# Kernel tuning notes

Measured on AMD Instinct MI355X. Metric: run time of the kernel, lower is better.

The kernel has to match this reference:

```python
import jax, jax.numpy as jnp
import numpy as np

B, S, D, H = 2, 2048, 1024, 16
DK = D // H  # 64


def setup_inputs() -> dict:
    key = jax.random.key(0)
    ks = jax.random.split(key, 4)
    scale = 1.0 / np.sqrt(D)
    return {
        "q_input": jax.random.normal(ks[0], (B, S, D), dtype=jnp.float32),
        "W_q": jax.random.normal(ks[1], (D, D), dtype=jnp.float32) * scale,
        "b_q": jnp.zeros((D,), dtype=jnp.float32),
        "W_k": jax.random.normal(ks[2], (D, D), dtype=jnp.float32) * scale,
        "b_k": jnp.zeros((D,), dtype=jnp.float32),
        "W_v": jax.random.normal(ks[3], (D, D), dtype=jnp.float32) * scale,
        "b_v": jnp.zeros((D,), dtype=jnp.float32),
    }


def reference(q_input, W_q, b_q, W_k, b_k, W_v, b_v):
    # Self-attention: k_input and v_input default to q_input in the torch module.
    # nn.Linear computes x @ W.T + b
    q = q_input @ W_q.T + b_q
    k = q_input @ W_k.T + b_k
    v = q_input @ W_v.T + b_v

    # [B,S,D] -> [B,H,S,DK]
    def split_heads(x):
        return x.reshape(B, S, H, DK).transpose(0, 2, 1, 3)

    qh, kh, vh = split_heads(q), split_heads(k), split_heads(v)

    # scores [B,H,S,S]; causal mask added BEFORE scaling (as in source; -inf invariant)
    scores = jnp.einsum("bhqd,bhkd->bhqk", qh, kh)
    causal = jnp.tril(jnp.ones((S, S), dtype=bool))
    scores = jnp.where(causal[None, None], scores, -jnp.inf)
    scores = scores / jnp.sqrt(jnp.float32(DK))
    probs = jax.nn.softmax(scores, axis=-1)
    z = jnp.einsum("bhqk,bhkd->bhqd", probs, vh)  # [B,H,S,DK]
    # [B,H,S,DK] -> [B,S,H,DK] -> [B,S,D]
    return z.transpose(0, 2, 1, 3).reshape(B, S, D)
```

## Files before the change

kernel.cpp:

```cpp
#include <hip/hip_runtime.h>
#include <hip/hip_bf16.h>
#include <stdint.h>

typedef __attribute__((ext_vector_type(8))) short short8;
typedef __attribute__((ext_vector_type(4))) short short4v;
typedef __attribute__((ext_vector_type(4))) float f32x4;

#define B_ 2
#define S_ 2048
#define D_ 1024
#define H_ 16
#define DK_ 64
#define M_ (B_*S_)

#define WS_QKV   0
#define WS_XB    12582912
#define WS_WB    16777216

#define QSCALE (0.125f * 1.44269504088896f)

#define GLL16(g, l) __builtin_amdgcn_global_load_lds( \
    (const __attribute__((address_space(1))) void*)(g), \
    (__attribute__((address_space(3))) void*)(l), 16, 0, 0)

#define WAIT_VM0 asm volatile("s_waitcnt vmcnt(0)" ::: "memory")
#define BARRIER_RAW asm volatile("s_barrier" ::: "memory")

static __device__ __forceinline__ short f2bf(float f){
  union { float f; unsigned u; } x; x.f = f;
  unsigned r = x.u + 0x7fff + ((x.u >> 16) & 1);
  return (short)(r >> 16);
}

__global__ __launch_bounds__(256) void cvt_bf16(
    const float* __restrict__ X,  const float* __restrict__ Wq,
    const float* __restrict__ Wk, const float* __restrict__ Wv,
    short* __restrict__ ws)
{
  const int z = blockIdx.z;
  const float* src; short* dst; int n;
  if (z == 0)      { src = X;  dst = ws + WS_XB;               n = M_*D_; }
  else if (z == 1) { src = Wq; dst = ws + WS_WB;               n = D_*D_; }
  else if (z == 2) { src = Wk; dst = ws + WS_WB + D_*D_;       n = D_*D_; }
  else             { src = Wv; dst = ws + WS_WB + 2*(D_*D_);   n = D_*D_; }
  const int stride = gridDim.x * blockDim.x * 4;
  for (int i = (blockIdx.x * blockDim.x + threadIdx.x) * 4; i < n; i += stride) {
    float4 v = *(const float4*)(src + i);
    short4v o;
    o.x = f2bf(v.x); o.y = f2bf(v.y); o.z = f2bf(v.z); o.w = f2bf(v.w);
    *(short4v*)(dst + i) = o;
  }
}

__global__ __launch_bounds__(256, 3) void qkv_gemm(
    const short* __restrict__ ws_in,
    const float* __restrict__ bq, const float* __restrict__ bk,
    const float* __restrict__ bv, short* __restrict__ qkv)
{
  const int z = blockIdx.z;
  const short* X  = ws_in + WS_XB;
  const short* Wm = ws_in + WS_WB + (size_t)z * (D_*D_);
  const float* bias = (z==0) ? bq : (z==1) ? bk : bv;
  short* out = qkv + (size_t)z * (M_*D_);

  __shared__ short lds[17408];

  const int t = threadIdx.x;
  const int w = t >> 6, lane = t & 63;
  const int quad = lane >> 4, l16 = lane & 15;
  const int wm = w & 1, wn = w >> 1;
  const int m0 = blockIdx.y * 128, n0 = blockIdx.x * 128;

  const int lr = lane >> 2, lc = lane & 3;
  const int csrc = lc ^ (lr & 3);
  const size_t arow0 = (size_t)(m0 + w*16     + lr) * D_ + csrc*8;
  const size_t arow1 = (size_t)(m0 + (w+4)*16 + lr) * D_ + csrc*8;
  const size_t brow0 = (size_t)(n0 + w*16     + lr) * D_ + csrc*8;
  const size_t brow1 = (size_t)(n0 + (w+4)*16 + lr) * D_ + csrc*8;

  f32x4 acc[4][4];
  #pragma unroll
  for (int i=0;i<4;i++)
    #pragma unroll
    for (int j=0;j<4;j++) acc[i][j] = (f32x4){0.f,0.f,0.f,0.f};

  GLL16(X  + arow0, lds + (w*16)*32);
  GLL16(X  + arow1, lds + ((w+4)*16)*32);
  GLL16(Wm + brow0, lds + 8192 + (w*16)*32);
  GLL16(Wm + brow1, lds + 8192 + ((w+4)*16)*32);

  const int ca = quad ^ (l16 & 3);
  int cur = 0;
  for (int kk = 0; kk < 32; kk++) {
    WAIT_VM0;
    BARRIER_RAW;
    const int nxt = cur ^ 1;
    if (kk < 31) {
      const int ko = (kk+1)*32;
      short* An = lds + nxt*4096;
      short* Bn = lds + 8192 + nxt*4096;
      GLL16(X  + arow0 + ko, An + (w*16)*32);
      GLL16(X  + arow1 + ko, An + ((w+4)*16)*32);
      GLL16(Wm + brow0 + ko, Bn + (w*16)*32);
      GLL16(Wm + brow1 + ko, Bn + ((w+4)*16)*32);
    }
    const short* Ac = lds + cur*4096;
    const short* Bc = lds + 8192 + cur*4096;
    short8 af[4], bfr[4];
    #pragma unroll
    for (int mt=0;mt<4;mt++)
      af[mt] = *(const short8*)(Ac + (wm*64 + mt*16 + l16)*32 + ca*8);
    #pragma unroll
    for (int nt=0;nt<4;nt++)
      bfr[nt] = *(const short8*)(Bc + (wn*64 + nt*16 + l16)*32 + ca*8);
    if (z != 2) {
      #pragma unroll
      for (int mt=0;mt<4;mt++)
        #pragma unroll
        for (int nt=0;nt<4;nt++)
          acc[mt][nt] = __builtin_amdgcn_mfma_f32_16x16x32_bf16(af[mt], bfr[nt], acc[mt][nt], 0,0,0);
    } else {
      #pragma unroll
      for (int nt=0;nt<4;nt++)
        #pragma unroll
        for (int mt=0;mt<4;mt++)
          acc[nt][mt] = __builtin_amdgcn_mfma_f32_16x16x32_bf16(bfr[nt], af[mt], acc[nt][mt], 0,0,0);
    }
    cur = nxt;
  }

  __syncthreads();

  if (z != 2) {
    const float scale = (z==0) ? QSCALE : 1.0f;
    #pragma unroll
    for (int nt=0;nt<4;nt++){
      const int col_l = wn*64 + nt*16 + l16;
      const float bvv = bias[n0 + col_l];
      #pragma unroll
      for (int mt=0;mt<4;mt++)
        #pragma unroll
        for (int i=0;i<4;i++){
          const int row_l = wm*64 + mt*16 + quad*4 + i;
          lds[row_l*136 + col_l] = f2bf((acc[mt][nt][i] + bvv) * scale);
        }
    }
    __syncthreads();
    #pragma unroll
    for (int k=0;k<8;k++){
      const int cid = k*256 + t;
      const int row = cid >> 4, cc = cid & 15;
      short8 vv = *(const short8*)(lds + row*136 + cc*8);
      const int m = m0 + row, bidx = m >> 11, s = m & 2047;
      const int n = n0 + cc*8, h = n >> 6, dd = n & 63;
      *(short8*)(out + (((size_t)(bidx*H_ + h))*S_ + s)*DK_ + dd) = vv;
    }
  } else {
    #pragma unroll
    for (int nt=0;nt<4;nt++)
      #pragma unroll
      for (int i=0;i<4;i++){
        const int n_l = wn*64 + nt*16 + quad*4 + i;
        const float bvv = bias[n0 + n_l];
        #pragma unroll
        for (int mt=0;mt<4;mt++){
          const int m_l = wm*64 + mt*16 + l16;
          lds[n_l*136 + m_l] = f2bf(acc[nt][mt][i] + bvv);
        }
      }
    __syncthreads();
    #pragma unroll
    for (int k=0;k<8;k++){
      const int cid = k*256 + t;
      const int rowN = cid >> 4, cc = cid & 15;
      short8 vv = *(const short8*)(lds + rowN*136 + cc*8);
      const int n = n0 + rowN, h = n >> 6, dd = n & 63;
      const int m = m0 + cc*8, bidx = m >> 11, s0 = m & 2047;
      *(short8*)(out + (((size_t)(bidx*H_ + h))*DK_ + dd)*S_ + s0) = vv;
    }
  }
}

__global__ __launch_bounds__(256, 2) void attn(
    const short* __restrict__ qkv, float* __restrict__ out)
{
  const int bh = blockIdx.y;
  const int qt = (gridDim.x - 1) - blockIdx.x;
  const short* Q  = qkv + (size_t)bh * (S_*DK_);
  const short* K  = Q + (size_t)(M_*D_);
  const short* VT = qkv + (size_t)(2*M_*D_) + (size_t)bh * (DK_*S_);

  __shared__ short Qs[8192];
  __shared__ short Kbuf[2][4096];
  __shared__ short Vbuf[2][4096];
  __shared__ short Ps[8192];

  const int t = threadIdx.x;
  const int w = t >> 6, lane = t & 63;
  const int quad = lane >> 4, l16 = lane & 15;
  const int sw = l16 & 7;
  const int lr = lane >> 3, lc = lane & 7;
  const int csrc = lc ^ lr;

  #pragma unroll
  for (int p=0;p<4;p++){
    const int rb = (p*4 + w)*8;
    GLL16(Q + (size_t)(qt*128 + rb + lr)*DK_ + csrc*8, Qs + rb*64);
  }
  {
    #pragma unroll
    for (int j=0;j<2;j++){
      const int rb = (j*4 + w)*8;
      GLL16(K  + (size_t)(rb + lr)*DK_ + csrc*8, &Kbuf[0][0] + rb*64);
      GLL16(VT + (size_t)(rb + lr)*S_  + csrc*8, &Vbuf[0][0] + rb*64);
    }
  }

  f32x4 o[2][4];
  float lsum[2][4];
  #pragma unroll
  for (int mt=0;mt<2;mt++){
    #pragma unroll
    for (int nd=0;nd<4;nd++) o[mt][nd] = (f32x4){0.f,0.f,0.f,0.f};
    #pragma unroll
    for (int i=0;i<4;i++) lsum[mt][i] = 0.f;
  }

  short8 aq[2][2];
  const int nkt = 2*qt + 2;
  int cur = 0;
  for (int kt = 0; kt < nkt; kt++){
    WAIT_VM0;
    BARRIER_RAW;
    const int nxt = cur ^ 1;
    if (kt + 1 < nkt) {
      const int kb2 = (kt+1)*64;
      short* Kn = &Kbuf[nxt][0];
      short* Vn = &Vbuf[nxt][0];
      #pragma unroll
      for (int j=0;j<2;j++){
        const int rb = (j*4 + w)*8;
        GLL16(K  + (size_t)(kb2 + rb + lr)*DK_ + csrc*8, Kn + rb*64);
        GLL16(VT + (size_t)(rb + lr)*S_ + kb2 + csrc*8,  Vn + rb*64);
      }
    }
    if (kt == 0) {
      #pragma unroll
      for (int kc=0;kc<2;kc++){
        const int xch = (kc*4 + quad) ^ sw;
        #pragma unroll
        for (int mt=0;mt<2;mt++)
          aq[kc][mt] = *(const short8*)(Qs + (w*32 + mt*16 + l16)*64 + xch*8);
      }
    }
    const short* Kc = &Kbuf[cur][0];
    const short* Vc = &Vbuf[cur][0];
    const int kb = kt*64;

    f32x4 sc[2][4];
    #pragma unroll
    for (int mt=0;mt<2;mt++)
      #pragma unroll
      for (int ntk=0;ntk<4;ntk++) sc[mt][ntk] = (f32x4){0.f,0.f,0.f,0.f};
    #pragma unroll
    for (int kc=0;kc<2;kc++){
      const int xch = (kc*4 + quad) ^ sw;
      short8 bk8[4];
      #pragma unroll
      for (int ntk=0;ntk<4;ntk++)
        bk8[ntk] = *(const short8*)(Kc + (ntk*16 + l16)*64 + xch*8);
      #pragma unroll
      for (int mt=0;mt<2;mt++)
        #pragma unroll
        for (int ntk=0;ntk<4;ntk++)
          sc[mt][ntk] = __builtin_amdgcn_mfma_f32_16x16x32_bf16(aq[kc][mt], bk8[ntk], sc[mt][ntk], 0,0,0);
    }

    const int q0w = qt*128 + w*32;
    if (kb + 63 > q0w) {
      #pragma unroll
      for (int mt=0;mt<2;mt++)
        #pragma unroll
        for (int ntk=0;ntk<4;ntk++)
          #pragma unroll
          for (int i=0;i<4;i++){
            const int qg = q0w + mt*16 + quad*4 + i;
            const int kg = kb + ntk*16 + l16;
            if (kg > qg) sc[mt][ntk][i] = -3.0e38f;
          }
    }

    #pragma unroll
    for (int mt=0;mt<2;mt++){
      #pragma unroll
      for (int i=0;i<4;i++){
        float p0 = __builtin_amdgcn_exp2f(sc[mt][0][i]);
        float p1 = __builtin_amdgcn_exp2f(sc[mt][1][i]);
        float p2 = __builtin_amdgcn_exp2f(sc[mt][2][i]);
        float p3 = __builtin_amdgcn_exp2f(sc[mt][3][i]);
        lsum[mt][i] += (p0+p1) + (p2+p3);
        const int prow = w*32 + mt*16 + quad*4 + i;
        const int off = prow*8 + (l16&7) + (l16>>3)*1024;
        Ps[ 1024*0 + off ] = f2bf(p0);
        Ps[ 1024*2 + off ] = f2bf(p1);
        Ps[ 1024*4 + off ] = f2bf(p2);
        Ps[ 1024*6 + off ] = f2bf(p3);
      }
    }
    asm volatile("" ::: "memory");

    #pragma unroll
    for (int kc=0;kc<2;kc++){
      const int ch  = kc*4 + quad;
      const int xch = ch ^ sw;
      short8 pa[2], vb[4];
      #pragma unroll
      for (int mt=0;mt<2;mt++)
        pa[mt] = *(const short8*)(Ps + (ch*128 + w*32 + mt*16 + l16)*8);
      #pragma unroll
      for (int nd=0;nd<4;nd++)
        vb[nd] = *(const short8*)(Vc + (nd*16 + l16)*64 + xch*8);
      #pragma unroll
      for (int mt=0;mt<2;mt++)
        #pragma unroll
        for (int nd=0;nd<4;nd++)
          o[mt][nd] = __builtin_amdgcn_mfma_f32_16x16x32_bf16(pa[mt], vb[nd], o[mt][nd], 0,0,0);
    }
    cur = nxt;
  }

  const int bb = bh >> 4, h = bh & 15;
  #pragma unroll
  for (int mt=0;mt<2;mt++)
    #pragma unroll
    for (int i=0;i<4;i++){
      float rs = lsum[mt][i];
      #pragma unroll
      for (int off=1; off<16; off<<=1)
        rs += __shfl_xor(rs, off, 64);
      lsum[mt][i] = 1.0f / rs;
    }
  #pragma unroll
  for (int mt=0;mt<2;mt++)
    #pragma unroll
    for (int nd=0;nd<4;nd++)
      #pragma unroll
      for (int i=0;i<4;i++){
        const int q = qt*128 + w*32 + mt*16 + quad*4 + i;
        const int d = nd*16 + l16;
        out[ ((size_t)bb*S_ + q)*D_ + h*DK_ + d ] = o[mt][nd][i] * lsum[mt][i];
      }
}

extern "C" void kernel_launch(void* const* d_in, const int* in_sizes, int n_in,
                              void* d_out, int out_size, void* d_ws, size_t ws_size,
                              hipStream_t stream)
{
  (void)in_sizes; (void)n_in; (void)out_size; (void)ws_size;
  const float* X  = (const float*)d_in[0];
  const float* Wq = (const float*)d_in[1];
  const float* bq = (const float*)d_in[2];
  const float* Wk = (const float*)d_in[3];
  const float* bk = (const float*)d_in[4];
  const float* Wv = (const float*)d_in[5];
  const float* bv = (const float*)d_in[6];
  short* ws  = (short*)d_ws;
  float* out = (float*)d_out;

  dim3 g0(1024, 1, 4);
  cvt_bf16<<<g0, dim3(256,1,1), 0, stream>>>(X, Wq, Wk, Wv, ws);
  dim3 g1(D_/128, M_/128, 3);
  qkv_gemm<<<g1, dim3(256,1,1), 0, stream>>>(ws, bq, bk, bv, ws + WS_QKV);
  dim3 g2(S_/128, B_*H_);
  attn<<<g2, dim3(256,1,1), 0, stream>>>(ws + WS_QKV, out);
}
```

Baseline: 190.9 us.

## Triple-buffer QKV GEMM loads and transpose score MFMA for packed P writes

The QKV projection GEMM moves from double to triple buffering in LDS, prefetching two K-steps ahead and waiting with vmcnt(4) so the next tile's loads stay in flight during compute. The attention kernel swaps the MFMA operand order for QK^T so each lane holds four consecutive keys of one query row. That lets P be written to LDS as packed 4-element vectors in a swizzled row layout, and the row sum reduces with two shuffles instead of four. This adds LDS use in the GEMM, which may lower occupancy, and adds a shuffle in the epilogue to broadcast the inverse sums.

```diff
diff --git a/kernel.cpp b/kernel.cpp
--- a/kernel.cpp
+++ b/kernel.cpp
@@ -24,6 +24,7 @@
     (__attribute__((address_space(3))) void*)(l), 16, 0, 0)
 
 #define WAIT_VM0 asm volatile("s_waitcnt vmcnt(0)" ::: "memory")
+#define WAIT_VM4 asm volatile("s_waitcnt vmcnt(4)" ::: "memory")
 #define BARRIER_RAW asm volatile("s_barrier" ::: "memory")
 
 static __device__ __forceinline__ short f2bf(float f){
@@ -63,7 +64,7 @@
   const float* bias = (z==0) ? bq : (z==1) ? bk : bv;
   short* out = qkv + (size_t)z * (M_*D_);
 
-  __shared__ short lds[17408];
+  __shared__ short lds[24576];
 
   const int t = threadIdx.x;
   const int w = t >> 6, lane = t & 63;
@@ -84,28 +85,32 @@
     #pragma unroll
     for (int j=0;j<4;j++) acc[i][j] = (f32x4){0.f,0.f,0.f,0.f};
 
-  GLL16(X  + arow0, lds + (w*16)*32);
-  GLL16(X  + arow1, lds + ((w+4)*16)*32);
-  GLL16(Wm + brow0, lds + 8192 + (w*16)*32);
-  GLL16(Wm + brow1, lds + 8192 + ((w+4)*16)*32);
+  #pragma unroll
+  for (int p=0;p<2;p++){
+    GLL16(X  + arow0 + p*32, lds + p*4096 + (w*16)*32);
+    GLL16(X  + arow1 + p*32, lds + p*4096 + ((w+4)*16)*32);
+    GLL16(Wm + brow0 + p*32, lds + 12288 + p*4096 + (w*16)*32);
+    GLL16(Wm + brow1 + p*32, lds + 12288 + p*4096 + ((w+4)*16)*32);
+  }
 
   const int ca = quad ^ (l16 & 3);
   int cur = 0;
   for (int kk = 0; kk < 32; kk++) {
-    WAIT_VM0;
+    if (kk < 31) { WAIT_VM4; }
+    else         { WAIT_VM0; }
     BARRIER_RAW;
-    const int nxt = cur ^ 1;
-    if (kk < 31) {
-      const int ko = (kk+1)*32;
-      short* An = lds + nxt*4096;
-      short* Bn = lds + 8192 + nxt*4096;
+    if (kk < 30) {
+      int slot = cur + 2; if (slot >= 3) slot -= 3;
+      const int ko = (kk+2)*32;
+      short* An = lds + slot*4096;
+      short* Bn = lds + 12288 + slot*4096;
       GLL16(X  + arow0 + ko, An + (w*16)*32);
       GLL16(X  + arow1 + ko, An + ((w+4)*16)*32);
       GLL16(Wm + brow0 + ko, Bn + (w*16)*32);
       GLL16(Wm + brow1 + ko, Bn + ((w+4)*16)*32);
     }
     const short* Ac = lds + cur*4096;
-    const short* Bc = lds + 8192 + cur*4096;
+    const short* Bc = lds + 12288 + cur*4096;
     short8 af[4], bfr[4];
     #pragma unroll
     for (int mt=0;mt<4;mt++)
@@ -126,7 +131,7 @@
         for (int mt=0;mt<4;mt++)
           acc[nt][mt] = __builtin_amdgcn_mfma_f32_16x16x32_bf16(bfr[nt], af[mt], acc[nt][mt], 0,0,0);
     }
-    cur = nxt;
+    cur = (cur==2) ? 0 : cur+1;
   }
 
   __syncthreads();
@@ -207,28 +212,28 @@
     const int rb = (p*4 + w)*8;
     GLL16(Q + (size_t)(qt*128 + rb + lr)*DK_ + csrc*8, Qs + rb*64);
   }
-  {
-    #pragma unroll
-    for (int j=0;j<2;j++){
-      const int rb = (j*4 + w)*8;
-      GLL16(K  + (size_t)(rb + lr)*DK_ + csrc*8, &Kbuf[0][0] + rb*64);
-      GLL16(VT + (size_t)(rb + lr)*S_  + csrc*8, &Vbuf[0][0] + rb*64);
-    }
+  #pragma unroll
+  for (int j=0;j<2;j++){
+    const int rb = (j*4 + w)*8;
+    GLL16(K  + (size_t)(rb + lr)*DK_ + csrc*8, &Kbuf[0][0] + rb*64);
+    GLL16(VT + (size_t)(rb + lr)*S_  + csrc*8, &Vbuf[0][0] + rb*64);
   }
 
   f32x4 o[2][4];
-  float lsum[2][4];
+  float lsum[2];
   #pragma unroll
   for (int mt=0;mt<2;mt++){
     #pragma unroll
     for (int nd=0;nd<4;nd++) o[mt][nd] = (f32x4){0.f,0.f,0.f,0.f};
-    #pragma unroll
-    for (int i=0;i<4;i++) lsum[mt][i] = 0.f;
-  }
-
-  short8 aq[2][2];
+    lsum[mt] = 0.f;
+  }
+
+  short8 bq[2][2];
   const int nkt = 2*qt + 2;
   int cur = 0;
+  const int pw_half = (quad & 1) * 4;
+  const int pw_ckb  = quad >> 1;
+
   for (int kt = 0; kt < nkt; kt++){
     WAIT_VM0;
     BARRIER_RAW;
@@ -250,73 +255,72 @@
         const int xch = (kc*4 + quad) ^ sw;
         #pragma unroll
         for (int mt=0;mt<2;mt++)
-          aq[kc][mt] = *(const short8*)(Qs + (w*32 + mt*16 + l16)*64 + xch*8);
+          bq[kc][mt] = *(const short8*)(Qs + (w*32 + mt*16 + l16)*64 + xch*8);
       }
     }
     const short* Kc = &Kbuf[cur][0];
     const short* Vc = &Vbuf[cur][0];
     const int kb = kt*64;
 
-    f32x4 sc[2][4];
-    #pragma unroll
-    for (int mt=0;mt<2;mt++)
-      #pragma unroll
-      for (int ntk=0;ntk<4;ntk++) sc[mt][ntk] = (f32x4){0.f,0.f,0.f,0.f};
+    f32x4 sc[4][2];
+    #pragma unroll
+    for (int ntk=0;ntk<4;ntk++)
+      #pragma unroll
+      for (int mt=0;mt<2;mt++) sc[ntk][mt] = (f32x4){0.f,0.f,0.f,0.f};
     #pragma unroll
     for (int kc=0;kc<2;kc++){
       const int xch = (kc*4 + quad) ^ sw;
-      short8 bk8[4];
+      short8 ak[4];
       #pragma unroll
       for (int ntk=0;ntk<4;ntk++)
-        bk8[ntk] = *(const short8*)(Kc + (ntk*16 + l16)*64 + xch*8);
-      #pragma unroll
-      for (int mt=0;mt<2;mt++)
-        #pragma unroll
-        for (int ntk=0;ntk<4;ntk++)
-          sc[mt][ntk] = __builtin_amdgcn_mfma_f32_16x16x32_bf16(aq[kc][mt], bk8[ntk], sc[mt][ntk], 0,0,0);
+        ak[ntk] = *(const short8*)(Kc + (ntk*16 + l16)*64 + xch*8);
+      #pragma unroll
+      for (int ntk=0;ntk<4;ntk++)
+        #pragma unroll
+        for (int mt=0;mt<2;mt++)
+          sc[ntk][mt] = __builtin_amdgcn_mfma_f32_16x16x32_bf16(ak[ntk], bq[kc][mt], sc[ntk][mt], 0,0,0);
     }
 
     const int q0w = qt*128 + w*32;
     if (kb + 63 > q0w) {
       #pragma unroll
-      for (int mt=0;mt<2;mt++)
-        #pragma unroll
-        for (int ntk=0;ntk<4;ntk++)
+      for (int ntk=0;ntk<4;ntk++)
+        #pragma unroll
+        for (int mt=0;mt<2;mt++){
+          const int qg = q0w + mt*16 + l16;
           #pragma unroll
           for (int i=0;i<4;i++){
-            const int qg = q0w + mt*16 + quad*4 + i;
-            const int kg = kb + ntk*16 + l16;
-            if (kg > qg) sc[mt][ntk][i] = -3.0e38f;
+            const int kg = kb + ntk*16 + quad*4 + i;
+            if (kg > qg) sc[ntk][mt][i] = -3.0e38f;
           }
+        }
     }
 
     #pragma unroll
     for (int mt=0;mt<2;mt++){
-      #pragma unroll
-      for (int i=0;i<4;i++){
-        float p0 = __builtin_amdgcn_exp2f(sc[mt][0][i]);
-        float p1 = __builtin_amdgcn_exp2f(sc[mt][1][i]);
-        float p2 = __builtin_amdgcn_exp2f(sc[mt][2][i]);
-        float p3 = __builtin_amdgcn_exp2f(sc[mt][3][i]);
-        lsum[mt][i] += (p0+p1) + (p2+p3);
-        const int prow = w*32 + mt*16 + quad*4 + i;
-        const int off = prow*8 + (l16&7) + (l16>>3)*1024;
-        Ps[ 1024*0 + off ] = f2bf(p0);
-        Ps[ 1024*2 + off ] = f2bf(p1);
-        Ps[ 1024*4 + off ] = f2bf(p2);
-        Ps[ 1024*6 + off ] = f2bf(p3);
+      const int r = w*32 + mt*16 + l16;
+      #pragma unroll
+      for (int ntk=0;ntk<4;ntk++){
+        float p0 = __builtin_amdgcn_exp2f(sc[ntk][mt][0]);
+        float p1 = __builtin_amdgcn_exp2f(sc[ntk][mt][1]);
+        float p2 = __builtin_amdgcn_exp2f(sc[ntk][mt][2]);
+        float p3 = __builtin_amdgcn_exp2f(sc[ntk][mt][3]);
+        lsum[mt] += (p0+p1) + (p2+p3);
+        short4v pk;
+        pk.x = f2bf(p0); pk.y = f2bf(p1); pk.z = f2bf(p2); pk.w = f2bf(p3);
+        const int slot = (ntk*2 + pw_ckb) ^ sw;
+        *(short4v*)(Ps + r*64 + slot*8 + pw_half) = pk;
       }
     }
     asm volatile("" ::: "memory");
 
     #pragma unroll
     for (int kc=0;kc<2;kc++){
-      const int ch  = kc*4 + quad;
-      const int xch = ch ^ sw;
+      const int xch = (kc*4 + quad) ^ sw;
       short8 pa[2], vb[4];
       #pragma unroll
       for (int mt=0;mt<2;mt++)
-        pa[mt] = *(const short8*)(Ps + (ch*128 + w*32 + mt*16 + l16)*8);
+        pa[mt] = *(const short8*)(Ps + (w*32 + mt*16 + l16)*64 + xch*8);
       #pragma unroll
       for (int nd=0;nd<4;nd++)
         vb[nd] = *(const short8*)(Vc + (nd*16 + l16)*64 + xch*8);
@@ -330,26 +334,27 @@
   }
 
   const int bb = bh >> 4, h = bh & 15;
-  #pragma unroll
-  for (int mt=0;mt<2;mt++)
+  float linv[2];
+  #pragma unroll
+  for (int mt=0;mt<2;mt++){
+    float rs = lsum[mt];
+    rs += __shfl_xor(rs, 16, 64);
+    rs += __shfl_xor(rs, 32, 64);
+    linv[mt] = 1.0f / rs;
+  }
+  #pragma unroll
+  for (int mt=0;mt<2;mt++){
     #pragma unroll
     for (int i=0;i<4;i++){
-      float rs = lsum[mt][i];
-      #pragma unroll
-      for (int off=1; off<16; off<<=1)
-        rs += __shfl_xor(rs, off, 64);
-      lsum[mt][i] = 1.0f / rs;
-    }
-  #pragma unroll
-  for (int mt=0;mt<2;mt++)
-    #pragma unroll
-    for (int nd=0;nd<4;nd++)
-      #pragma unroll
-      for (int i=0;i<4;i++){
-        const int q = qt*128 + w*32 + mt*16 + quad*4 + i;
+      const float lw = __shfl(linv[mt], (quad<<4) + (quad<<2) + i, 64);
+      const int q = qt*128 + w*32 + mt*16 + quad*4 + i;
+      #pragma unroll
+      for (int nd=0;nd<4;nd++){
         const int d = nd*16 + l16;
-        out[ ((size_t)bb*S_ + q)*D_ + h*DK_ + d ] = o[mt][nd][i] * lsum[mt][i];
-      }
+        out[ ((size_t)bb*S_ + q)*D_ + h*DK_ + d ] = o[mt][nd][i] * lw;
+      }
+    }
+  }
 }
 
 extern "C" void kernel_launch(void* const* d_in, const int* in_sizes, int n_in,
```

New measurement: 187.0 us. -2.1%, faster.
